# Kernel tuning notes

Hardware: AMD Instinct MI355X
Metric: run time of the kernel (lower is better)

## Reference

```python
import jax, jax.numpy as jnp
import numpy as np

N = 10000      # atoms
E = 160000     # edges (avg degree 16)
G = 20         # graphs
Z = 10         # num_elements
K = 64         # hidden scalar channels (hidden_irreps multiplicity)
NB = 8         # num_bessel
H = 64         # radial MLP width
LMAX = 3
LM = (LMAX + 1) ** 2   # 16 spherical-harmonic components
M = 16         # MLP_irreps width for final nonlinear readout
R_MAX = 5.0
AVG_NEIGH = 16.0
LS = np.array([l for l in range(LMAX + 1) for _ in range(2 * l + 1)])  # l index of each lm slot


def _sph(u):
    # real spherical harmonics up to l=3, 'component' normalization, on unit vectors u [E,3]
    x, y, z = u[:, 0], u[:, 1], u[:, 2]
    s3, s5, s15, s7 = 3.0 ** 0.5, 5.0 ** 0.5, 15.0 ** 0.5, 7.0 ** 0.5
    c31, c32, c33 = (21.0 / 8.0) ** 0.5, 105.0 ** 0.5, (35.0 / 8.0) ** 0.5
    Y = [jnp.ones_like(x),
         s3 * x, s3 * y, s3 * z,
         s15 * x * y, s15 * y * z, 0.5 * s5 * (3 * z * z - 1.0), s15 * x * z, 0.5 * s15 * (x * x - y * y),
         c33 * y * (3 * x * x - y * y), c32 * x * y * z, c31 * y * (5 * z * z - 1.0),
         0.5 * s7 * z * (5 * z * z - 3.0),
         c31 * x * (5 * z * z - 1.0), 0.5 * c32 * z * (x * x - y * y), c33 * x * (x * x - 3 * y * y)]
    return jnp.stack(Y, axis=-1)


def _radial(r):
    # Bessel radial basis with p=5 polynomial cutoff envelope
    u = r / R_MAX
    n = jnp.arange(1, NB + 1, dtype=r.dtype)
    bess = (2.0 / R_MAX) ** 0.5 * jnp.sin(n[None, :] * jnp.pi * u[:, None]) / r[:, None]
    env = jnp.where(u < 1.0, 1.0 - 21.0 * u ** 5 + 35.0 * u ** 6 - 15.0 * u ** 7, 0.0)
    return bess * env[:, None]


def _forward(node_attrs, positions, atomic_energies, W_embed, radial_W0, radial_W1, radial_W2, radial_W3, W_mix, Wz, W_out, w_read1, W_r1, w_r2, edge_index, batch):
    sender, receiver = edge_index[0], edge_index[1]
    vec = positions[receiver] - positions[sender]          # edge gather
    r = jnp.sqrt(jnp.sum(vec * vec, axis=-1) + 1e-12)
    Y = _sph(vec / r[:, None])                             # [E, 16]
    edge_feats = _radial(r)                                # [E, NB]
    node_e0 = node_attrs @ atomic_energies                 # [N]
    feats = node_attrs @ W_embed                           # node embedding [N, K]
    node_en = node_e0
    for t in range(2):  # num_interactions
        # radial MLP -> per-(channel,l) tensor-product weights
        h = edge_feats
        for W in (radial_W0[t], radial_W1[t], radial_W2[t]):
            h = jax.nn.silu(h @ W)
        Rw = (h @ radial_W3[t]).reshape(-1, K, LMAX + 1)[:, :, LS]   # [E, K, 16]
        # channelwise tensor product: sender feats x SH x radial weights
        msg = feats[sender][:, :, None] * Rw * Y[:, None, :]         # [E, K, 16]
        A = jax.ops.segment_sum(msg, receiver, num_segments=node_attrs.shape[0]) / AVG_NEIGH
        A = jnp.einsum('nkm,mkc->ncm', A, W_mix[t][LS])              # per-l linear channel mixing
        # equivariant product basis (correlation 3) -> invariant contractions with element-dep weights
        s1 = A[:, :, 0]
        inv2 = jnp.sum(A * A, axis=-1)
        b = (node_attrs @ Wz[t, 0]) * s1 + (node_attrs @ Wz[t, 1]) * inv2 + (node_attrs @ Wz[t, 2]) * (s1 * inv2)
        feats = b @ W_out[t]
        if t == 0:
            node_en = node_en + feats @ w_read1              # linear readout
        else:
            node_en = node_en + jax.nn.silu(feats @ W_r1) @ w_r2  # nonlinear readout
    return jax.ops.segment_sum(node_en, batch, num_segments=G)      # per-graph energies [G]


def setup_inputs():
    key = jax.random.key(0)
    ks = jax.random.split(key, 16)
    gn = lambda k, shape, fan: jax.random.normal(k, shape, dtype=jnp.float32) / (fan ** 0.5)
    species = jax.random.randint(ks[0], (N,), 0, Z)
    return {
        'node_attrs': jax.nn.one_hot(species, Z, dtype=jnp.float32),
        'positions': jax.random.normal(ks[1], (N, 3), dtype=jnp.float32) * 3.0,
        'edge_index': jax.random.randint(ks[2], (2, E), 0, N),
        'batch': jnp.sort(jax.random.randint(ks[3], (N,), 0, G)),
        'atomic_energies': jax.random.normal(ks[4], (Z,), dtype=jnp.float32),
        'W_embed': gn(ks[5], (Z, K), Z),
        'radial_W0': gn(ks[6], (2, NB, H), NB),
        'radial_W1': gn(ks[7], (2, H, H), H),
        'radial_W2': gn(ks[8], (2, H, H), H),
        'radial_W3': gn(ks[9], (2, H, K * (LMAX + 1)), H),
        'W_mix': gn(ks[10], (2, LMAX + 1, K, K), K),
        'Wz': gn(ks[11], (2, 3, Z, K), Z),
        'W_out': gn(ks[12], (2, K, K), K),
        'w_read1': gn(ks[13], (K,), K),
        'W_r1': gn(ks[14], (K, M), K),
        'w_r2': gn(ks[15], (M,), M),
    }


def reference(node_attrs, positions, edge_index, batch, atomic_energies, W_embed, radial_W0, radial_W1, radial_W2, radial_W3, W_mix, Wz, W_out, w_read1, W_r1, w_r2):
    return _forward(node_attrs, positions, atomic_energies, W_embed, radial_W0, radial_W1, radial_W2, radial_W3, W_mix, Wz, W_out, w_read1, W_r1, w_r2, edge_index, batch)
```

## Files before the change

kernel.cpp:

```cpp
#include <hip/hip_runtime.h>
#include <hip/hip_bf16.h>
#include <math.h>

#define NN 10000
#define NE 160000
#define NG 20
#define NZ 10
#define INV_AVG 0.0625f
#define PSTRIDE 76
#define NSTR 1040

typedef __attribute__((ext_vector_type(8))) short bf16x8;
typedef __attribute__((ext_vector_type(4))) float f32x4;
typedef __attribute__((ext_vector_type(4))) unsigned short u16x4;
typedef __attribute__((ext_vector_type(8))) unsigned short u16x8;

__device__ __forceinline__ float silu(float x) {
    return x * __builtin_amdgcn_rcpf(1.0f + __expf(-x));
}

__device__ __forceinline__ unsigned short f2b(float f) {
    union { float f; unsigned u; } v; v.f = f;
    unsigned r = v.u + 0x7FFF + ((v.u >> 16) & 1);
    return (unsigned short)(r >> 16);
}
__device__ __forceinline__ float b2f(unsigned short h) {
    union { unsigned u; float f; } v; v.u = ((unsigned)h) << 16; return v.f;
}

__global__ __launch_bounds__(256) void node_init(
    const float* __restrict__ attrs, const float* __restrict__ W_embed,
    const float* __restrict__ ae,
    float* __restrict__ feats, float* __restrict__ node_en)
{
    int gid = blockIdx.x * blockDim.x + threadIdx.x;
    if (gid >= NN * 64) return;
    int n = gid >> 6, k = gid & 63;
    float acc = 0.f;
#pragma unroll
    for (int z = 0; z < NZ; ++z) acc += attrs[n * NZ + z] * W_embed[z * 64 + k];
    feats[gid] = acc;
    if (k == 0) {
        float e0 = 0.f;
#pragma unroll
        for (int z = 0; z < NZ; ++z) e0 += attrs[n * NZ + z] * ae[z];
        node_en[n] = e0;
    }
}

__global__ __launch_bounds__(256) void csr_count(const int* __restrict__ ei, int* __restrict__ cnt)
{
    int e = blockIdx.x * 256 + threadIdx.x;
    if (e < NE) atomicAdd(&cnt[ei[NE + e]], 1);
}

__global__ __launch_bounds__(1024) void csr_scan(const int* __restrict__ cnt, int* __restrict__ row)
{
    __shared__ int part[1024];
    const int tid = threadIdx.x;
    const int base = tid * 10;
    int loc[10];
    int s = 0;
#pragma unroll
    for (int q = 0; q < 10; ++q) {
        int idx = base + q;
        int v = (idx < NN) ? cnt[idx] : 0;
        loc[q] = s; s += v;
    }
    part[tid] = s;
    __syncthreads();
    for (int off = 1; off < 1024; off <<= 1) {
        int v = (tid >= off) ? part[tid - off] : 0;
        __syncthreads();
        part[tid] += v;
        __syncthreads();
    }
    int pre = (tid > 0) ? part[tid - 1] : 0;
#pragma unroll
    for (int q = 0; q < 10; ++q) {
        int idx = base + q;
        if (idx < NN) row[idx] = pre + loc[q];
    }
    if (tid == 1023) row[NN] = part[1023];
}

__global__ __launch_bounds__(256) void csr_scatter(
    const int* __restrict__ ei, const int* __restrict__ row,
    int* __restrict__ cur, int* __restrict__ perm)
{
    int e = blockIdx.x * 256 + threadIdx.x;
    if (e < NE) {
        int r = ei[NE + e];
        int p = atomicAdd(&cur[r], 1);
        perm[row[r] + p] = e;
    }
}

__global__ __launch_bounds__(256) void w_prep(
    const float* __restrict__ rW0, const float* __restrict__ rW1,
    const float* __restrict__ rW2, const float* __restrict__ rW3,
    const float* __restrict__ Wmix,
    unsigned short* __restrict__ w0f, unsigned short* __restrict__ w1f,
    unsigned short* __restrict__ w2f, unsigned short* __restrict__ w3f,
    unsigned short* __restrict__ wmixf)
{
    int g = blockIdx.x * 256 + threadIdx.x;
    if (g < 4096) {
        int t = g >> 11, x = g & 2047;
        int nt = x >> 9, l = (x >> 3) & 63, j = x & 7;
        int k = (l >> 4) * 8 + j, c = nt * 16 + (l & 15);
        w0f[g] = (k < 8) ? f2b(rW0[t * 512 + k * 64 + c]) : (unsigned short)0;
    } else if (g < 20480) {
        int x0 = g - 4096;
        int t = x0 >> 13, x = x0 & 8191;
        int fidx = x >> 9, l = (x >> 3) & 63, j = x & 7;
        int kt = fidx >> 2, nt = fidx & 3;
        int k = kt * 32 + (l >> 4) * 8 + j, c = nt * 16 + (l & 15);
        w1f[x0] = f2b(rW1[t * 4096 + k * 64 + c]);
    } else if (g < 36864) {
        int x0 = g - 20480;
        int t = x0 >> 13, x = x0 & 8191;
        int fidx = x >> 9, l = (x >> 3) & 63, j = x & 7;
        int kt = fidx >> 2, nt = fidx & 3;
        int k = kt * 32 + (l >> 4) * 8 + j, c = nt * 16 + (l & 15);
        w2f[x0] = f2b(rW2[t * 4096 + k * 64 + c]);
    } else if (g < 69632) {
        int x0 = g - 36864;
        int t = x0 >> 14, x = x0 & 16383;
        int fidx = x >> 9, l = (x >> 3) & 63, j = x & 7;
        int kt = fidx >> 4, nt = fidx & 15;
        int k = kt * 32 + (l >> 4) * 8 + j, c = nt * 16 + (l & 15);
        w3f[x0] = f2b(rW3[t * 16384 + k * 256 + c]);
    } else if (g < 102400) {
        int x0 = g - 69632;
        int t = x0 >> 14;
        int x = x0 & 16383;
        int l = x >> 12;
        int xx = x & 4095;
        int f = xx >> 9, ll = (xx >> 3) & 63, j = xx & 7;
        int kt = f >> 2, ct = f & 3;
        int k = kt * 32 + (ll >> 4) * 8 + j, c = ct * 16 + (ll & 15);
        wmixf[x0] = f2b(Wmix[t * 16384 + l * 4096 + k * 64 + c]);
    }
}

__global__ __launch_bounds__(256) void edge_geom(
    const int* __restrict__ ei, const float* __restrict__ pos,
    const int* __restrict__ perm,
    unsigned short* __restrict__ ybg, unsigned short* __restrict__ ebg,
    int* __restrict__ snd_p)
{
    const int g = blockIdx.x * 256 + threadIdx.x;
    const int e = perm[g];
    const int snd = ei[e], rcv = ei[NE + e];
    snd_p[g] = snd;
    const float dx = pos[rcv * 3 + 0] - pos[snd * 3 + 0];
    const float dy = pos[rcv * 3 + 1] - pos[snd * 3 + 1];
    const float dz = pos[rcv * 3 + 2] - pos[snd * 3 + 2];
    const float r = sqrtf(dx * dx + dy * dy + dz * dz + 1e-12f);
    const float ir = 1.0f / r;
    const float x = dx * ir, y = dy * ir, z = dz * ir;
    const float xx = x * x, yy = y * y, zz = z * z;

    u16x8 ylo, yhi;
    ylo[0] = f2b(1.0f);
    ylo[1] = f2b(1.73205081f * x);
    ylo[2] = f2b(1.73205081f * y);
    ylo[3] = f2b(1.73205081f * z);
    ylo[4] = f2b(3.87298335f * x * y);
    ylo[5] = f2b(3.87298335f * y * z);
    ylo[6] = f2b(1.11803399f * (3.0f * zz - 1.0f));
    ylo[7] = f2b(3.87298335f * x * z);
    yhi[0] = f2b(1.93649167f * (xx - yy));
    yhi[1] = f2b(2.09165007f * y * (3.0f * xx - yy));
    yhi[2] = f2b(10.2469508f * x * y * z);
    yhi[3] = f2b(1.62018517f * y * (5.0f * zz - 1.0f));
    yhi[4] = f2b(1.32287566f * z * (5.0f * zz - 3.0f));
    yhi[5] = f2b(1.62018517f * x * (5.0f * zz - 1.0f));
    yhi[6] = f2b(5.12347538f * z * (xx - yy));
    yhi[7] = f2b(2.09165007f * x * (xx - 3.0f * yy));
    *(u16x8*)&ybg[(size_t)g * 16] = ylo;
    *(u16x8*)&ybg[(size_t)g * 16 + 8] = yhi;

    const float u = r * 0.2f;
    float env = 0.0f;
    if (u < 1.0f) {
        const float u2 = u * u, u5 = u2 * u2 * u;
        env = 1.0f - 21.0f * u5 + 35.0f * u5 * u - 15.0f * u5 * u2;
    }
    const float cb = 0.632455532f * ir * env;
    const float pu = 3.14159265358979f * u;
    u16x8 eb;
#pragma unroll
    for (int i = 0; i < 8; ++i) eb[i] = f2b(cb * __sinf((float)(i + 1) * pu));
    *(u16x8*)&ebg[(size_t)g * 8] = eb;
}

__global__ __launch_bounds__(256) void radial_fused(
    const unsigned short* __restrict__ ebg,
    const unsigned short* __restrict__ w0f,
    const unsigned short* __restrict__ w1f,
    const unsigned short* __restrict__ w2f,
    const unsigned short* __restrict__ w3f,
    unsigned short* __restrict__ rwb)
{
    __shared__ unsigned short sP[4][16 * PSTRIDE];
    const int w = threadIdx.x >> 6, lane = threadIdx.x & 63;
    const int tIdx = blockIdx.x * 4 + w;
    const int lg = lane >> 4, e16 = lane & 15;
    unsigned short* buf = &sP[w][0];

    const size_t g0 = (size_t)tIdx * 16;
    f32x4 c[4];

    bf16x8 a1 = {0, 0, 0, 0, 0, 0, 0, 0};
    if (lg == 0) a1 = *(const bf16x8*)&ebg[(g0 + e16) * 8];
#pragma unroll
    for (int nt = 0; nt < 4; ++nt) {
        const bf16x8 b = *(const bf16x8*)&w0f[nt * 512 + lane * 8];
        c[nt] = __builtin_amdgcn_mfma_f32_16x16x32_bf16(b, a1, (f32x4){0.f, 0.f, 0.f, 0.f}, 0, 0, 0);
    }
#pragma unroll
    for (int nt = 0; nt < 4; ++nt) {
        u16x4 o;
#pragma unroll
        for (int jj = 0; jj < 4; ++jj) o[jj] = f2b(silu(c[nt][jj]));
        *(u16x4*)&buf[e16 * PSTRIDE + nt * 16 + lg * 4] = o;
    }

    {
        const bf16x8 ak0 = *(const bf16x8*)&buf[e16 * PSTRIDE + lg * 8];
        const bf16x8 ak1 = *(const bf16x8*)&buf[e16 * PSTRIDE + 32 + lg * 8];
#pragma unroll
        for (int nt = 0; nt < 4; ++nt) {
            const bf16x8 b0 = *(const bf16x8*)&w1f[nt * 512 + lane * 8];
            const bf16x8 b1 = *(const bf16x8*)&w1f[(4 + nt) * 512 + lane * 8];
            f32x4 acc = __builtin_amdgcn_mfma_f32_16x16x32_bf16(b0, ak0, (f32x4){0.f, 0.f, 0.f, 0.f}, 0, 0, 0);
            c[nt] = __builtin_amdgcn_mfma_f32_16x16x32_bf16(b1, ak1, acc, 0, 0, 0);
        }
    }
#pragma unroll
    for (int nt = 0; nt < 4; ++nt) {
        u16x4 o;
#pragma unroll
        for (int jj = 0; jj < 4; ++jj) o[jj] = f2b(silu(c[nt][jj]));
        *(u16x4*)&buf[e16 * PSTRIDE + nt * 16 + lg * 4] = o;
    }

    {
        const bf16x8 ak0 = *(const bf16x8*)&buf[e16 * PSTRIDE + lg * 8];
        const bf16x8 ak1 = *(const bf16x8*)&buf[e16 * PSTRIDE + 32 + lg * 8];
#pragma unroll
        for (int nt = 0; nt < 4; ++nt) {
            const bf16x8 b0 = *(const bf16x8*)&w2f[nt * 512 + lane * 8];
            const bf16x8 b1 = *(const bf16x8*)&w2f[(4 + nt) * 512 + lane * 8];
            f32x4 acc = __builtin_amdgcn_mfma_f32_16x16x32_bf16(b0, ak0, (f32x4){0.f, 0.f, 0.f, 0.f}, 0, 0, 0);
            c[nt] = __builtin_amdgcn_mfma_f32_16x16x32_bf16(b1, ak1, acc, 0, 0, 0);
        }
    }
#pragma unroll
    for (int nt = 0; nt < 4; ++nt) {
        u16x4 o;
#pragma unroll
        for (int jj = 0; jj < 4; ++jj) o[jj] = f2b(silu(c[nt][jj]));
        *(u16x4*)&buf[e16 * PSTRIDE + nt * 16 + lg * 4] = o;
    }

    {
        const bf16x8 h0 = *(const bf16x8*)&buf[e16 * PSTRIDE + lg * 8];
        const bf16x8 h1 = *(const bf16x8*)&buf[e16 * PSTRIDE + 32 + lg * 8];
#pragma unroll 4
        for (int nt = 0; nt < 16; ++nt) {
            const bf16x8 b0 = *(const bf16x8*)&w3f[nt * 512 + lane * 8];
            const bf16x8 b1 = *(const bf16x8*)&w3f[(16 + nt) * 512 + lane * 8];
            f32x4 cc = __builtin_amdgcn_mfma_f32_16x16x32_bf16(b0, h0, (f32x4){0.f, 0.f, 0.f, 0.f}, 0, 0, 0);
            cc = __builtin_amdgcn_mfma_f32_16x16x32_bf16(b1, h1, cc, 0, 0, 0);
            u16x4 o;
#pragma unroll
            for (int jj = 0; jj < 4; ++jj) o[jj] = f2b(cc[jj]);
            *(u16x4*)&rwb[(g0 + e16) * 256 + nt * 16 + lg * 4] = o;
        }
    }
}

#define EDGE_FMA(rv_, f_, y0_, y1_) do { \
    const float p0 = (f_) * b2f((rv_)[0]), p1 = (f_) * b2f((rv_)[1]); \
    const float p2 = (f_) * b2f((rv_)[2]), p3 = (f_) * b2f((rv_)[3]); \
    acc[0]  += p0 * b2f((y0_)[0]); \
    acc[1]  += p1 * b2f((y0_)[1]);  acc[2]  += p1 * b2f((y0_)[2]);  acc[3]  += p1 * b2f((y0_)[3]); \
    acc[4]  += p2 * b2f((y0_)[4]);  acc[5]  += p2 * b2f((y0_)[5]);  acc[6]  += p2 * b2f((y0_)[6]); \
    acc[7]  += p2 * b2f((y0_)[7]);  acc[8]  += p2 * b2f((y1_)[0]); \
    acc[9]  += p3 * b2f((y1_)[1]);  acc[10] += p3 * b2f((y1_)[2]);  acc[11] += p3 * b2f((y1_)[3]); \
    acc[12] += p3 * b2f((y1_)[4]);  acc[13] += p3 * b2f((y1_)[5]);  acc[14] += p3 * b2f((y1_)[6]); \
    acc[15] += p3 * b2f((y1_)[7]); \
} while (0)

#define LOADBATCH(rv_, f_, y0_, y1_, gb_) do { \
    _Pragma("unroll") \
    for (int j = 0; j < 4; ++j) { \
        const int gg = (gb_) + j; \
        rv_[j] = *(const u16x4*)&rwb[(size_t)gg * 256 + lane * 4]; \
        f_[j]  = feats_in[(size_t)snd_p[gg] * 64 + lane]; \
        y0_[j] = *(const u16x8*)&ybg[(size_t)gg * 16]; \
        y1_[j] = *(const u16x8*)&ybg[(size_t)gg * 16 + 8]; \
    } } while (0)

#define FMABATCH(rv_, f_, y0_, y1_) do { \
    _Pragma("unroll") \
    for (int j = 0; j < 4; ++j) EDGE_FMA(rv_[j], f_[j], y0_[j], y1_[j]); } while (0)

__global__ __launch_bounds__(256) void msg_accum(
    const unsigned short* __restrict__ rwb, const unsigned short* __restrict__ ybg,
    const int* __restrict__ row, const int* __restrict__ snd_p,
    const float* __restrict__ feats_in, unsigned short* __restrict__ Abp)
{
    const int w = threadIdx.x >> 6, lane = threadIdx.x & 63;
    const int n = blockIdx.x * 4 + w;
    const int beg = row[n], end = row[n + 1];

    float acc[16];
#pragma unroll
    for (int m = 0; m < 16; ++m) acc[m] = 0.f;

    u16x4 rvA[4], rvB[4];
    float fA[4], fB[4];
    u16x8 y0A[4], y0B[4], y1A[4], y1B[4];

    const int nb = (end - beg) >> 2;
    if (nb > 0) {
        LOADBATCH(rvA, fA, y0A, y1A, beg);
        int b = 0;
        while (true) {
            if (b + 1 < nb) LOADBATCH(rvB, fB, y0B, y1B, beg + (b + 1) * 4);
            FMABATCH(rvA, fA, y0A, y1A);
            ++b;
            if (b >= nb) break;
            if (b + 1 < nb) LOADBATCH(rvA, fA, y0A, y1A, beg + (b + 1) * 4);
            FMABATCH(rvB, fB, y0B, y1B);
            ++b;
            if (b >= nb) break;
        }
    }
    for (int g = beg + nb * 4; g < end; ++g) {
        const u16x4 rv = *(const u16x4*)&rwb[(size_t)g * 256 + lane * 4];
        const float f = feats_in[(size_t)snd_p[g] * 64 + lane];
        const u16x8 y0 = *(const u16x8*)&ybg[(size_t)g * 16];
        const u16x8 y1 = *(const u16x8*)&ybg[(size_t)g * 16 + 8];
        EDGE_FMA(rv, f, y0, y1);
    }

#pragma unroll
    for (int m = 0; m < 16; ++m)
        Abp[(size_t)m * 640000 + (size_t)n * 64 + lane] = f2b(acc[m] * INV_AVG);
}

__global__ __launch_bounds__(256) void einsum_gate(
    const unsigned short* __restrict__ Abp,
    const unsigned short* __restrict__ wmixf,
    const float* __restrict__ attrs,
    const float* __restrict__ Wz, const float* __restrict__ Wout,
    const float* __restrict__ wread1, const float* __restrict__ Wr1,
    const float* __restrict__ wr2,
    float* __restrict__ feats_out, float* __restrict__ node_en, int t)
{
    __shared__ unsigned short sNew[16 * NSTR];
    __shared__ float sF[4][64];
    const int w = threadIdx.x >> 6, lane = threadIdx.x & 63;
    const int lg = lane >> 4, n16 = lane & 15;
    const size_t node0 = (size_t)blockIdx.x * 16;

#pragma unroll
    for (int q = 0; q < 4; ++q) {
        const int m = w * 4 + q;
        const int l = (m == 0) ? 0 : (m < 4) ? 1 : (m < 9) ? 2 : 3;
        const unsigned short* Am = Abp + (size_t)m * 640000;
        const bf16x8 a0 = *(const bf16x8*)&Am[(node0 + n16) * 64 + lg * 8];
        const bf16x8 a1 = *(const bf16x8*)&Am[(node0 + n16) * 64 + 32 + lg * 8];
        const unsigned short* Wl = wmixf + l * 4096;
#pragma unroll
        for (int ct = 0; ct < 4; ++ct) {
            const bf16x8 b0 = *(const bf16x8*)&Wl[ct * 512 + lane * 8];
            const bf16x8 b1 = *(const bf16x8*)&Wl[(4 + ct) * 512 + lane * 8];
            f32x4 cc = __builtin_amdgcn_mfma_f32_16x16x32_bf16(b0, a0, (f32x4){0.f, 0.f, 0.f, 0.f}, 0, 0, 0);
            cc = __builtin_amdgcn_mfma_f32_16x16x32_bf16(b1, a1, cc, 0, 0, 0);
            u16x4 o;
#pragma unroll
            for (int jj = 0; jj < 4; ++jj) o[jj] = f2b(cc[jj]);
            *(u16x4*)&sNew[n16 * NSTR + m * 64 + ct * 16 + lg * 4] = o;
        }
    }
    __syncthreads();

    for (int qq = 0; qq < 4; ++qq) {
        const int nl = w * 4 + qq;
        const int n = (int)node0 + nl;

        float vals[16];
#pragma unroll
        for (int m = 0; m < 16; ++m)
            vals[m] = b2f(sNew[nl * NSTR + m * 64 + lane]);

        const float s1 = vals[0];
        float inv2 = 0.f;
#pragma unroll
        for (int m = 0; m < 16; ++m) inv2 += vals[m] * vals[m];

        float z0 = 0.f, z1 = 0.f, z2 = 0.f;
#pragma unroll
        for (int zz = 0; zz < NZ; ++zz) {
            const float a = attrs[n * NZ + zz];
            z0 += a * Wz[(t * 3 + 0) * 640 + zz * 64 + lane];
            z1 += a * Wz[(t * 3 + 1) * 640 + zz * 64 + lane];
            z2 += a * Wz[(t * 3 + 2) * 640 + zz * 64 + lane];
        }
        const float b = z0 * s1 + z1 * inv2 + z2 * (s1 * inv2);

        sF[w][lane] = b;
        float fnew = 0.f;
#pragma unroll 8
        for (int j = 0; j < 64; ++j) fnew += sF[w][j] * Wout[j * 64 + lane];
        feats_out[(size_t)n * 64 + lane] = fnew;

        if (t == 0) {
            float v = fnew * wread1[lane];
#pragma unroll
            for (int off = 32; off > 0; off >>= 1) v += __shfl_down(v, off, 64);
            if (lane == 0) node_en[n] += v;
        } else {
            sF[w][lane] = fnew;
            if (lane < 16) {
                float a = 0.f;
#pragma unroll 8
                for (int j = 0; j < 64; ++j) a += sF[w][j] * Wr1[j * 16 + lane];
                float vv = silu(a) * wr2[lane];
                vv += __shfl_down(vv, 8, 64);
                vv += __shfl_down(vv, 4, 64);
                vv += __shfl_down(vv, 2, 64);
                vv += __shfl_down(vv, 1, 64);
                if (lane == 0) node_en[n] += vv;
            }
        }
    }
}

__global__ __launch_bounds__(1024) void final_reduce(
    const float* __restrict__ node_en, const int* __restrict__ batch,
    float* __restrict__ out)
{
    __shared__ float sg[NG];
    if (threadIdx.x < NG) sg[threadIdx.x] = 0.f;
    __syncthreads();
    for (int n = threadIdx.x; n < NN; n += 1024)
        atomicAdd(&sg[batch[n]], node_en[n]);
    __syncthreads();
    if (threadIdx.x < NG) out[threadIdx.x] = sg[threadIdx.x];
}

extern "C" void kernel_launch(void* const* d_in, const int* in_sizes, int n_in,
                              void* d_out, int out_size, void* d_ws, size_t ws_size,
                              hipStream_t stream) {
    const float* attrs   = (const float*)d_in[0];
    const float* pos     = (const float*)d_in[1];
    const int*   ei      = (const int*)d_in[2];
    const int*   batch   = (const int*)d_in[3];
    const float* ae      = (const float*)d_in[4];
    const float* W_embed = (const float*)d_in[5];
    const float* rW0     = (const float*)d_in[6];
    const float* rW1     = (const float*)d_in[7];
    const float* rW2     = (const float*)d_in[8];
    const float* rW3     = (const float*)d_in[9];
    const float* Wmix    = (const float*)d_in[10];
    const float* Wz      = (const float*)d_in[11];
    const float* Wout    = (const float*)d_in[12];
    const float* wread1  = (const float*)d_in[13];
    const float* Wr1     = (const float*)d_in[14];
    const float* wr2     = (const float*)d_in[15];
    float* out = (float*)d_out;

    char* ws = (char*)d_ws;
    unsigned short* rwb  = (unsigned short*)(ws);
    unsigned short* ybg  = (unsigned short*)(ws + 81920000);
    unsigned short* ebg  = (unsigned short*)(ws + 87040000);
    float* feats0        = (float*)(ws + 89600000);
    float* feats1        = (float*)(ws + 92160000);
    unsigned short* Abp  = (unsigned short*)(ws + 94720000);
    unsigned short* w0f  = (unsigned short*)(ws + 115200000);
    unsigned short* w1f  = (unsigned short*)(ws + 115208192);
    unsigned short* w2f  = (unsigned short*)(ws + 115240960);
    unsigned short* w3f  = (unsigned short*)(ws + 115273728);
    unsigned short* wmixf= (unsigned short*)(ws + 115339264);
    int* cnt             = (int*)(ws + 115404800);
    int* cur             = (int*)(ws + 115445760);
    int* rowst           = (int*)(ws + 115486720);
    int* perm            = (int*)(ws + 115527696);
    int* snd_p           = (int*)(ws + 116167696);
    float* node_en       = (float*)(ws + 116807696);

    hipMemsetAsync(cnt, 0, 81920, stream);

    node_init<<<2500, 256, 0, stream>>>(attrs, W_embed, ae, feats0, node_en);

    csr_count<<<625, 256, 0, stream>>>(ei, cnt);
    csr_scan<<<1, 1024, 0, stream>>>(cnt, rowst);
    csr_scatter<<<625, 256, 0, stream>>>(ei, rowst, cur, perm);

    w_prep<<<400, 256, 0, stream>>>(rW0, rW1, rW2, rW3, Wmix,
                                    w0f, w1f, w2f, w3f, wmixf);
    edge_geom<<<625, 256, 0, stream>>>(ei, pos, perm, ybg, ebg, snd_p);

    for (int t = 0; t < 2; ++t) {
        radial_fused<<<2500, 256, 0, stream>>>(
            ebg, w0f + t * 2048, w1f + t * 8192, w2f + t * 8192, w3f + t * 16384, rwb);
        msg_accum<<<2500, 256, 0, stream>>>(
            rwb, ybg, rowst, snd_p, (t == 0) ? feats0 : feats1, Abp);
        einsum_gate<<<625, 256, 0, stream>>>(
            Abp, wmixf + t * 16384, attrs, Wz, Wout + t * 4096,
            wread1, Wr1, wr2,
            (t == 0) ? feats1 : feats0, node_en, t);
    }
    final_reduce<<<1, 1024, 0, stream>>>(node_en, batch, out);
}
```

Before: 260.4 us.

## Co-schedule second-layer radial MLP with first message pass; merge setup kernels

The second interaction's radial MLP depends only on edge geometry, so it now runs inside the same launch as the first message accumulation, alternating blocks between the memory-bound gather and the MFMA-bound radial tile. This needs a second radial-weight buffer, which roughly doubles that workspace region. Setup kernels are also merged (node init with CSR count, scan with weight prep) to cut launch count and serialization. The aim is to overlap compute-heavy and memory-heavy work and remove small-kernel gaps, at the cost of extra workspace traffic and mixed-occupancy blocks.

```diff
diff --git a/kernel.cpp b/kernel.cpp
--- a/kernel.cpp
+++ b/kernel.cpp
@@ -28,75 +28,183 @@
     union { unsigned u; float f; } v; v.u = ((unsigned)h) << 16; return v.f;
 }
 
-__global__ __launch_bounds__(256) void node_init(
+__device__ __forceinline__ void radial_tile(
+    int tIdx, int lane, unsigned short* buf,
+    const unsigned short* __restrict__ ebg,
+    const unsigned short* __restrict__ w0f, const unsigned short* __restrict__ w1f,
+    const unsigned short* __restrict__ w2f, const unsigned short* __restrict__ w3f,
+    unsigned short* __restrict__ rwb)
+{
+    const int lg = lane >> 4, e16 = lane & 15;
+    const size_t g0 = (size_t)tIdx * 16;
+    f32x4 c[4];
+
+    bf16x8 a1 = {0, 0, 0, 0, 0, 0, 0, 0};
+    if (lg == 0) a1 = *(const bf16x8*)&ebg[(g0 + e16) * 8];
+#pragma unroll
+    for (int nt = 0; nt < 4; ++nt) {
+        const bf16x8 b = *(const bf16x8*)&w0f[nt * 512 + lane * 8];
+        c[nt] = __builtin_amdgcn_mfma_f32_16x16x32_bf16(b, a1, (f32x4){0.f, 0.f, 0.f, 0.f}, 0, 0, 0);
+    }
+#pragma unroll
+    for (int nt = 0; nt < 4; ++nt) {
+        u16x4 o;
+#pragma unroll
+        for (int jj = 0; jj < 4; ++jj) o[jj] = f2b(silu(c[nt][jj]));
+        *(u16x4*)&buf[e16 * PSTRIDE + nt * 16 + lg * 4] = o;
+    }
+
+    {
+        const bf16x8 ak0 = *(const bf16x8*)&buf[e16 * PSTRIDE + lg * 8];
+        const bf16x8 ak1 = *(const bf16x8*)&buf[e16 * PSTRIDE + 32 + lg * 8];
+#pragma unroll
+        for (int nt = 0; nt < 4; ++nt) {
+            const bf16x8 b0 = *(const bf16x8*)&w1f[nt * 512 + lane * 8];
+            const bf16x8 b1 = *(const bf16x8*)&w1f[(4 + nt) * 512 + lane * 8];
+            f32x4 acc = __builtin_amdgcn_mfma_f32_16x16x32_bf16(b0, ak0, (f32x4){0.f, 0.f, 0.f, 0.f}, 0, 0, 0);
+            c[nt] = __builtin_amdgcn_mfma_f32_16x16x32_bf16(b1, ak1, acc, 0, 0, 0);
+        }
+    }
+#pragma unroll
+    for (int nt = 0; nt < 4; ++nt) {
+        u16x4 o;
+#pragma unroll
+        for (int jj = 0; jj < 4; ++jj) o[jj] = f2b(silu(c[nt][jj]));
+        *(u16x4*)&buf[e16 * PSTRIDE + nt * 16 + lg * 4] = o;
+    }
+
+    {
+        const bf16x8 ak0 = *(const bf16x8*)&buf[e16 * PSTRIDE + lg * 8];
+        const bf16x8 ak1 = *(const bf16x8*)&buf[e16 * PSTRIDE + 32 + lg * 8];
+#pragma unroll
+        for (int nt = 0; nt < 4; ++nt) {
+            const bf16x8 b0 = *(const bf16x8*)&w2f[nt * 512 + lane * 8];
+            const bf16x8 b1 = *(const bf16x8*)&w2f[(4 + nt) * 512 + lane * 8];
+            f32x4 acc = __builtin_amdgcn_mfma_f32_16x16x32_bf16(b0, ak0, (f32x4){0.f, 0.f, 0.f, 0.f}, 0, 0, 0);
+            c[nt] = __builtin_amdgcn_mfma_f32_16x16x32_bf16(b1, ak1, acc, 0, 0, 0);
+        }
+    }
+#pragma unroll
+    for (int nt = 0; nt < 4; ++nt) {
+        u16x4 o;
+#pragma unroll
+        for (int jj = 0; jj < 4; ++jj) o[jj] = f2b(silu(c[nt][jj]));
+        *(u16x4*)&buf[e16 * PSTRIDE + nt * 16 + lg * 4] = o;
+    }
+
+    {
+        const bf16x8 h0 = *(const bf16x8*)&buf[e16 * PSTRIDE + lg * 8];
+        const bf16x8 h1 = *(const bf16x8*)&buf[e16 * PSTRIDE + 32 + lg * 8];
+#pragma unroll 4
+        for (int nt = 0; nt < 16; ++nt) {
+            const bf16x8 b0 = *(const bf16x8*)&w3f[nt * 512 + lane * 8];
+            const bf16x8 b1 = *(const bf16x8*)&w3f[(16 + nt) * 512 + lane * 8];
+            f32x4 cc = __builtin_amdgcn_mfma_f32_16x16x32_bf16(b0, h0, (f32x4){0.f, 0.f, 0.f, 0.f}, 0, 0, 0);
+            cc = __builtin_amdgcn_mfma_f32_16x16x32_bf16(b1, h1, cc, 0, 0, 0);
+            u16x4 o;
+#pragma unroll
+            for (int jj = 0; jj < 4; ++jj) o[jj] = f2b(cc[jj]);
+            *(u16x4*)&rwb[(g0 + e16) * 256 + nt * 16 + lg * 4] = o;
+        }
+    }
+}
+
+#define EDGE_FMA(rv_, f_, y0_, y1_) do { \
+    const float p0 = (f_) * b2f((rv_)[0]), p1 = (f_) * b2f((rv_)[1]); \
+    const float p2 = (f_) * b2f((rv_)[2]), p3 = (f_) * b2f((rv_)[3]); \
+    acc[0]  += p0 * b2f((y0_)[0]); \
+    acc[1]  += p1 * b2f((y0_)[1]);  acc[2]  += p1 * b2f((y0_)[2]);  acc[3]  += p1 * b2f((y0_)[3]); \
+    acc[4]  += p2 * b2f((y0_)[4]);  acc[5]  += p2 * b2f((y0_)[5]);  acc[6]  += p2 * b2f((y0_)[6]); \
+    acc[7]  += p2 * b2f((y0_)[7]);  acc[8]  += p2 * b2f((y1_)[0]); \
+    acc[9]  += p3 * b2f((y1_)[1]);  acc[10] += p3 * b2f((y1_)[2]);  acc[11] += p3 * b2f((y1_)[3]); \
+    acc[12] += p3 * b2f((y1_)[4]);  acc[13] += p3 * b2f((y1_)[5]);  acc[14] += p3 * b2f((y1_)[6]); \
+    acc[15] += p3 * b2f((y1_)[7]); \
+} while (0)
+
+#define LOADBATCH(rv_, f_, y0_, y1_, gb_) do { \
+    _Pragma("unroll") \
+    for (int j = 0; j < 4; ++j) { \
+        const int gg = (gb_) + j; \
+        rv_[j] = *(const u16x4*)&rwb[(size_t)gg * 256 + lane * 4]; \
+        f_[j]  = feats_in[(size_t)snd_p[gg] * 64 + lane]; \
+        y0_[j] = *(const u16x8*)&ybg[(size_t)gg * 16]; \
+        y1_[j] = *(const u16x8*)&ybg[(size_t)gg * 16 + 8]; \
+    } } while (0)
+
+#define FMABATCH(rv_, f_, y0_, y1_) do { \
+    _Pragma("unroll") \
+    for (int j = 0; j < 4; ++j) EDGE_FMA(rv_[j], f_[j], y0_[j], y1_[j]); } while (0)
+
+__device__ __forceinline__ void msg_node(
+    int n, int lane,
+    const unsigned short* __restrict__ rwb, const unsigned short* __restrict__ ybg,
+    const int* __restrict__ row, const int* __restrict__ snd_p,
+    const float* __restrict__ feats_in, unsigned short* __restrict__ Abp)
+{
+    const int beg = row[n], end = row[n + 1];
+
+    float acc[16];
+#pragma unroll
+    for (int m = 0; m < 16; ++m) acc[m] = 0.f;
+
+    u16x4 rvA[4], rvB[4];
+    float fA[4], fB[4];
+    u16x8 y0A[4], y0B[4], y1A[4], y1B[4];
+
+    const int nb = (end - beg) >> 2;
+    if (nb > 0) {
+        LOADBATCH(rvA, fA, y0A, y1A, beg);
+        int b = 0;
+        while (true) {
+            if (b + 1 < nb) LOADBATCH(rvB, fB, y0B, y1B, beg + (b + 1) * 4);
+            FMABATCH(rvA, fA, y0A, y1A);
+            ++b;
+            if (b >= nb) break;
+            if (b + 1 < nb) LOADBATCH(rvA, fA, y0A, y1A, beg + (b + 1) * 4);
+            FMABATCH(rvB, fB, y0B, y1B);
+            ++b;
+            if (b >= nb) break;
+        }
+    }
+    for (int g = beg + nb * 4; g < end; ++g) {
+        const u16x4 rv = *(const u16x4*)&rwb[(size_t)g * 256 + lane * 4];
+        const float f = feats_in[(size_t)snd_p[g] * 64 + lane];
+        const u16x8 y0 = *(const u16x8*)&ybg[(size_t)g * 16];
+        const u16x8 y1 = *(const u16x8*)&ybg[(size_t)g * 16 + 8];
+        EDGE_FMA(rv, f, y0, y1);
+    }
+
+#pragma unroll
+    for (int m = 0; m < 16; ++m)
+        Abp[(size_t)m * 640000 + (size_t)n * 64 + lane] = f2b(acc[m] * INV_AVG);
+}
+
+__global__ __launch_bounds__(256) void init_count(
     const float* __restrict__ attrs, const float* __restrict__ W_embed,
-    const float* __restrict__ ae,
-    float* __restrict__ feats, float* __restrict__ node_en)
-{
-    int gid = blockIdx.x * blockDim.x + threadIdx.x;
-    if (gid >= NN * 64) return;
-    int n = gid >> 6, k = gid & 63;
-    float acc = 0.f;
-#pragma unroll
-    for (int z = 0; z < NZ; ++z) acc += attrs[n * NZ + z] * W_embed[z * 64 + k];
-    feats[gid] = acc;
-    if (k == 0) {
-        float e0 = 0.f;
-#pragma unroll
-        for (int z = 0; z < NZ; ++z) e0 += attrs[n * NZ + z] * ae[z];
-        node_en[n] = e0;
-    }
-}
-
-__global__ __launch_bounds__(256) void csr_count(const int* __restrict__ ei, int* __restrict__ cnt)
-{
-    int e = blockIdx.x * 256 + threadIdx.x;
-    if (e < NE) atomicAdd(&cnt[ei[NE + e]], 1);
-}
-
-__global__ __launch_bounds__(1024) void csr_scan(const int* __restrict__ cnt, int* __restrict__ row)
-{
-    __shared__ int part[1024];
-    const int tid = threadIdx.x;
-    const int base = tid * 10;
-    int loc[10];
-    int s = 0;
-#pragma unroll
-    for (int q = 0; q < 10; ++q) {
-        int idx = base + q;
-        int v = (idx < NN) ? cnt[idx] : 0;
-        loc[q] = s; s += v;
-    }
-    part[tid] = s;
-    __syncthreads();
-    for (int off = 1; off < 1024; off <<= 1) {
-        int v = (tid >= off) ? part[tid - off] : 0;
-        __syncthreads();
-        part[tid] += v;
-        __syncthreads();
-    }
-    int pre = (tid > 0) ? part[tid - 1] : 0;
-#pragma unroll
-    for (int q = 0; q < 10; ++q) {
-        int idx = base + q;
-        if (idx < NN) row[idx] = pre + loc[q];
-    }
-    if (tid == 1023) row[NN] = part[1023];
-}
-
-__global__ __launch_bounds__(256) void csr_scatter(
-    const int* __restrict__ ei, const int* __restrict__ row,
-    int* __restrict__ cur, int* __restrict__ perm)
-{
-    int e = blockIdx.x * 256 + threadIdx.x;
-    if (e < NE) {
-        int r = ei[NE + e];
-        int p = atomicAdd(&cur[r], 1);
-        perm[row[r] + p] = e;
-    }
-}
-
-__global__ __launch_bounds__(256) void w_prep(
+    const float* __restrict__ ae, const int* __restrict__ ei,
+    float* __restrict__ feats, float* __restrict__ node_en, int* __restrict__ cnt)
+{
+    if (blockIdx.x < 2500) {
+        int gid = blockIdx.x * 256 + threadIdx.x;
+        int n = gid >> 6, k = gid & 63;
+        float acc = 0.f;
+#pragma unroll
+        for (int z = 0; z < NZ; ++z) acc += attrs[n * NZ + z] * W_embed[z * 64 + k];
+        feats[gid] = acc;
+        if (k == 0) {
+            float e0 = 0.f;
+#pragma unroll
+            for (int z = 0; z < NZ; ++z) e0 += attrs[n * NZ + z] * ae[z];
+            node_en[n] = e0;
+        }
+    } else {
+        int e = (blockIdx.x - 2500) * 256 + threadIdx.x;
+        if (e < NE) atomicAdd(&cnt[ei[NE + e]], 1);
+    }
+}
+
+__global__ __launch_bounds__(1024) void scan_prep(
+    const int* __restrict__ cnt, int* __restrict__ row,
     const float* __restrict__ rW0, const float* __restrict__ rW1,
     const float* __restrict__ rW2, const float* __restrict__ rW3,
     const float* __restrict__ Wmix,
@@ -104,43 +212,84 @@
     unsigned short* __restrict__ w2f, unsigned short* __restrict__ w3f,
     unsigned short* __restrict__ wmixf)
 {
-    int g = blockIdx.x * 256 + threadIdx.x;
-    if (g < 4096) {
-        int t = g >> 11, x = g & 2047;
-        int nt = x >> 9, l = (x >> 3) & 63, j = x & 7;
-        int k = (l >> 4) * 8 + j, c = nt * 16 + (l & 15);
-        w0f[g] = (k < 8) ? f2b(rW0[t * 512 + k * 64 + c]) : (unsigned short)0;
-    } else if (g < 20480) {
-        int x0 = g - 4096;
-        int t = x0 >> 13, x = x0 & 8191;
-        int fidx = x >> 9, l = (x >> 3) & 63, j = x & 7;
-        int kt = fidx >> 2, nt = fidx & 3;
-        int k = kt * 32 + (l >> 4) * 8 + j, c = nt * 16 + (l & 15);
-        w1f[x0] = f2b(rW1[t * 4096 + k * 64 + c]);
-    } else if (g < 36864) {
-        int x0 = g - 20480;
-        int t = x0 >> 13, x = x0 & 8191;
-        int fidx = x >> 9, l = (x >> 3) & 63, j = x & 7;
-        int kt = fidx >> 2, nt = fidx & 3;
-        int k = kt * 32 + (l >> 4) * 8 + j, c = nt * 16 + (l & 15);
-        w2f[x0] = f2b(rW2[t * 4096 + k * 64 + c]);
-    } else if (g < 69632) {
-        int x0 = g - 36864;
-        int t = x0 >> 14, x = x0 & 16383;
-        int fidx = x >> 9, l = (x >> 3) & 63, j = x & 7;
-        int kt = fidx >> 4, nt = fidx & 15;
-        int k = kt * 32 + (l >> 4) * 8 + j, c = nt * 16 + (l & 15);
-        w3f[x0] = f2b(rW3[t * 16384 + k * 256 + c]);
-    } else if (g < 102400) {
-        int x0 = g - 69632;
-        int t = x0 >> 14;
-        int x = x0 & 16383;
-        int l = x >> 12;
-        int xx = x & 4095;
-        int f = xx >> 9, ll = (xx >> 3) & 63, j = xx & 7;
-        int kt = f >> 2, ct = f & 3;
-        int k = kt * 32 + (ll >> 4) * 8 + j, c = ct * 16 + (ll & 15);
-        wmixf[x0] = f2b(Wmix[t * 16384 + l * 4096 + k * 64 + c]);
+    if (blockIdx.x == 0) {
+        __shared__ int part[1024];
+        const int tid = threadIdx.x;
+        const int base = tid * 10;
+        int loc[10];
+        int s = 0;
+#pragma unroll
+        for (int q = 0; q < 10; ++q) {
+            int idx = base + q;
+            int v = (idx < NN) ? cnt[idx] : 0;
+            loc[q] = s; s += v;
+        }
+        part[tid] = s;
+        __syncthreads();
+        for (int off = 1; off < 1024; off <<= 1) {
+            int v = (tid >= off) ? part[tid - off] : 0;
+            __syncthreads();
+            part[tid] += v;
+            __syncthreads();
+        }
+        int pre = (tid > 0) ? part[tid - 1] : 0;
+#pragma unroll
+        for (int q = 0; q < 10; ++q) {
+            int idx = base + q;
+            if (idx < NN) row[idx] = pre + loc[q];
+        }
+        if (tid == 1023) row[NN] = part[1023];
+    } else {
+        int g = (blockIdx.x - 1) * 1024 + threadIdx.x;
+        if (g < 4096) {
+            int t = g >> 11, x = g & 2047;
+            int nt = x >> 9, l = (x >> 3) & 63, j = x & 7;
+            int k = (l >> 4) * 8 + j, c = nt * 16 + (l & 15);
+            w0f[g] = (k < 8) ? f2b(rW0[t * 512 + k * 64 + c]) : (unsigned short)0;
+        } else if (g < 20480) {
+            int x0 = g - 4096;
+            int t = x0 >> 13, x = x0 & 8191;
+            int fidx = x >> 9, l = (x >> 3) & 63, j = x & 7;
+            int kt = fidx >> 2, nt = fidx & 3;
+            int k = kt * 32 + (l >> 4) * 8 + j, c = nt * 16 + (l & 15);
+            w1f[x0] = f2b(rW1[t * 4096 + k * 64 + c]);
+        } else if (g < 36864) {
+            int x0 = g - 20480;
+            int t = x0 >> 13, x = x0 & 8191;
+            int fidx = x >> 9, l = (x >> 3) & 63, j = x & 7;
+            int kt = fidx >> 2, nt = fidx & 3;
+            int k = kt * 32 + (l >> 4) * 8 + j, c = nt * 16 + (l & 15);
+            w2f[x0] = f2b(rW2[t * 4096 + k * 64 + c]);
+        } else if (g < 69632) {
+            int x0 = g - 36864;
+            int t = x0 >> 14, x = x0 & 16383;
+            int fidx = x >> 9, l = (x >> 3) & 63, j = x & 7;
+            int kt = fidx >> 4, nt = fidx & 15;
+            int k = kt * 32 + (l >> 4) * 8 + j, c = nt * 16 + (l & 15);
+            w3f[x0] = f2b(rW3[t * 16384 + k * 256 + c]);
+        } else if (g < 102400) {
+            int x0 = g - 69632;
+            int t = x0 >> 14;
+            int x = x0 & 16383;
+            int l = x >> 12;
+            int xx = x & 4095;
+            int f = xx >> 9, ll = (xx >> 3) & 63, j = xx & 7;
+            int kt = f >> 2, ct = f & 3;
+            int k = kt * 32 + (ll >> 4) * 8 + j, c = ct * 16 + (ll & 15);
+            wmixf[x0] = f2b(Wmix[t * 16384 + l * 4096 + k * 64 + c]);
+        }
+    }
+}
+
+__global__ __launch_bounds__(256) void csr_scatter(
+    const int* __restrict__ ei, const int* __restrict__ row,
+    int* __restrict__ cur, int* __restrict__ perm)
+{
+    int e = blockIdx.x * 256 + threadIdx.x;
+    if (e < NE) {
+        int r = ei[NE + e];
+        int p = atomicAdd(&cur[r], 1);
+        perm[row[r] + p] = e;
     }
 }
 
@@ -206,108 +355,27 @@
 {
     __shared__ unsigned short sP[4][16 * PSTRIDE];
     const int w = threadIdx.x >> 6, lane = threadIdx.x & 63;
-    const int tIdx = blockIdx.x * 4 + w;
-    const int lg = lane >> 4, e16 = lane & 15;
-    unsigned short* buf = &sP[w][0];
-
-    const size_t g0 = (size_t)tIdx * 16;
-    f32x4 c[4];
-
-    bf16x8 a1 = {0, 0, 0, 0, 0, 0, 0, 0};
-    if (lg == 0) a1 = *(const bf16x8*)&ebg[(g0 + e16) * 8];
-#pragma unroll
-    for (int nt = 0; nt < 4; ++nt) {
-        const bf16x8 b = *(const bf16x8*)&w0f[nt * 512 + lane * 8];
-        c[nt] = __builtin_amdgcn_mfma_f32_16x16x32_bf16(b, a1, (f32x4){0.f, 0.f, 0.f, 0.f}, 0, 0, 0);
-    }
-#pragma unroll
-    for (int nt = 0; nt < 4; ++nt) {
-        u16x4 o;
-#pragma unroll
-        for (int jj = 0; jj < 4; ++jj) o[jj] = f2b(silu(c[nt][jj]));
-        *(u16x4*)&buf[e16 * PSTRIDE + nt * 16 + lg * 4] = o;
-    }
-
-    {
-        const bf16x8 ak0 = *(const bf16x8*)&buf[e16 * PSTRIDE + lg * 8];
-        const bf16x8 ak1 = *(const bf16x8*)&buf[e16 * PSTRIDE + 32 + lg * 8];
-#pragma unroll
-        for (int nt = 0; nt < 4; ++nt) {
-            const bf16x8 b0 = *(const bf16x8*)&w1f[nt * 512 + lane * 8];
-            const bf16x8 b1 = *(const bf16x8*)&w1f[(4 + nt) * 512 + lane * 8];
-            f32x4 acc = __builtin_amdgcn_mfma_f32_16x16x32_bf16(b0, ak0, (f32x4){0.f, 0.f, 0.f, 0.f}, 0, 0, 0);
-            c[nt] = __builtin_amdgcn_mfma_f32_16x16x32_bf16(b1, ak1, acc, 0, 0, 0);
-        }
-    }
-#pragma unroll
-    for (int nt = 0; nt < 4; ++nt) {
-        u16x4 o;
-#pragma unroll
-        for (int jj = 0; jj < 4; ++jj) o[jj] = f2b(silu(c[nt][jj]));
-        *(u16x4*)&buf[e16 * PSTRIDE + nt * 16 + lg * 4] = o;
-    }
-
-    {
-        const bf16x8 ak0 = *(const bf16x8*)&buf[e16 * PSTRIDE + lg * 8];
-        const bf16x8 ak1 = *(const bf16x8*)&buf[e16 * PSTRIDE + 32 + lg * 8];
-#pragma unroll
-        for (int nt = 0; nt < 4; ++nt) {
-            const bf16x8 b0 = *(const bf16x8*)&w2f[nt * 512 + lane * 8];
-            const bf16x8 b1 = *(const bf16x8*)&w2f[(4 + nt) * 512 + lane * 8];
-            f32x4 acc = __builtin_amdgcn_mfma_f32_16x16x32_bf16(b0, ak0, (f32x4){0.f, 0.f, 0.f, 0.f}, 0, 0, 0);
-            c[nt] = __builtin_amdgcn_mfma_f32_16x16x32_bf16(b1, ak1, acc, 0, 0, 0);
-        }
-    }
-#pragma unroll
-    for (int nt = 0; nt < 4; ++nt) {
-        u16x4 o;
-#pragma unroll
-        for (int jj = 0; jj < 4; ++jj) o[jj] = f2b(silu(c[nt][jj]));
-        *(u16x4*)&buf[e16 * PSTRIDE + nt * 16 + lg * 4] = o;
-    }
-
-    {
-        const bf16x8 h0 = *(const bf16x8*)&buf[e16 * PSTRIDE + lg * 8];
-        const bf16x8 h1 = *(const bf16x8*)&buf[e16 * PSTRIDE + 32 + lg * 8];
-#pragma unroll 4
-        for (int nt = 0; nt < 16; ++nt) {
-            const bf16x8 b0 = *(const bf16x8*)&w3f[nt * 512 + lane * 8];
-            const bf16x8 b1 = *(const bf16x8*)&w3f[(16 + nt) * 512 + lane * 8];
-            f32x4 cc = __builtin_amdgcn_mfma_f32_16x16x32_bf16(b0, h0, (f32x4){0.f, 0.f, 0.f, 0.f}, 0, 0, 0);
-            cc = __builtin_amdgcn_mfma_f32_16x16x32_bf16(b1, h1, cc, 0, 0, 0);
-            u16x4 o;
-#pragma unroll
-            for (int jj = 0; jj < 4; ++jj) o[jj] = f2b(cc[jj]);
-            *(u16x4*)&rwb[(g0 + e16) * 256 + nt * 16 + lg * 4] = o;
-        }
-    }
-}
-
-#define EDGE_FMA(rv_, f_, y0_, y1_) do { \
-    const float p0 = (f_) * b2f((rv_)[0]), p1 = (f_) * b2f((rv_)[1]); \
-    const float p2 = (f_) * b2f((rv_)[2]), p3 = (f_) * b2f((rv_)[3]); \
-    acc[0]  += p0 * b2f((y0_)[0]); \
-    acc[1]  += p1 * b2f((y0_)[1]);  acc[2]  += p1 * b2f((y0_)[2]);  acc[3]  += p1 * b2f((y0_)[3]); \
-    acc[4]  += p2 * b2f((y0_)[4]);  acc[5]  += p2 * b2f((y0_)[5]);  acc[6]  += p2 * b2f((y0_)[6]); \
-    acc[7]  += p2 * b2f((y0_)[7]);  acc[8]  += p2 * b2f((y1_)[0]); \
-    acc[9]  += p3 * b2f((y1_)[1]);  acc[10] += p3 * b2f((y1_)[2]);  acc[11] += p3 * b2f((y1_)[3]); \
-    acc[12] += p3 * b2f((y1_)[4]);  acc[13] += p3 * b2f((y1_)[5]);  acc[14] += p3 * b2f((y1_)[6]); \
-    acc[15] += p3 * b2f((y1_)[7]); \
-} while (0)
-
-#define LOADBATCH(rv_, f_, y0_, y1_, gb_) do { \
-    _Pragma("unroll") \
-    for (int j = 0; j < 4; ++j) { \
-        const int gg = (gb_) + j; \
-        rv_[j] = *(const u16x4*)&rwb[(size_t)gg * 256 + lane * 4]; \
-        f_[j]  = feats_in[(size_t)snd_p[gg] * 64 + lane]; \
-        y0_[j] = *(const u16x8*)&ybg[(size_t)gg * 16]; \
-        y1_[j] = *(const u16x8*)&ybg[(size_t)gg * 16 + 8]; \
-    } } while (0)
-
-#define FMABATCH(rv_, f_, y0_, y1_) do { \
-    _Pragma("unroll") \
-    for (int j = 0; j < 4; ++j) EDGE_FMA(rv_[j], f_[j], y0_[j], y1_[j]); } while (0)
+    radial_tile(blockIdx.x * 4 + w, lane, &sP[w][0], ebg, w0f, w1f, w2f, w3f, rwb);
+}
+
+__global__ __launch_bounds__(256) void msg_radial(
+    const unsigned short* __restrict__ rwb0, const unsigned short* __restrict__ ybg,
+    const int* __restrict__ row, const int* __restrict__ snd_p,
+    const float* __restrict__ feats_in, unsigned short* __restrict__ Abp,
+    const unsigned short* __restrict__ ebg,
+    const unsigned short* __restrict__ w0f, const unsigned short* __restrict__ w1f,
+    const unsigned short* __restrict__ w2f, const unsigned short* __restrict__ w3f,
+    unsigned short* __restrict__ rwb1)
+{
+    __shared__ unsigned short sP[4][16 * PSTRIDE];
+    const int w = threadIdx.x >> 6, lane = threadIdx.x & 63;
+    const int sub = blockIdx.x >> 1;
+    if ((blockIdx.x & 1) == 0) {
+        msg_node(sub * 4 + w, lane, rwb0, ybg, row, snd_p, feats_in, Abp);
+    } else {
+        radial_tile(sub * 4 + w, lane, &sP[w][0], ebg, w0f, w1f, w2f, w3f, rwb1);
+    }
+}
 
 __global__ __launch_bounds__(256) void msg_accum(
     const unsigned short* __restrict__ rwb, const unsigned short* __restrict__ ybg,
@@ -315,43 +383,7 @@
     const float* __restrict__ feats_in, unsigned short* __restrict__ Abp)
 {
     const int w = threadIdx.x >> 6, lane = threadIdx.x & 63;
-    const int n = blockIdx.x * 4 + w;
-    const int beg = row[n], end = row[n + 1];
-
-    float acc[16];
-#pragma unroll
-    for (int m = 0; m < 16; ++m) acc[m] = 0.f;
-
-    u16x4 rvA[4], rvB[4];
-    float fA[4], fB[4];
-    u16x8 y0A[4], y0B[4], y1A[4], y1B[4];
-
-    const int nb = (end - beg) >> 2;
-    if (nb > 0) {
-        LOADBATCH(rvA, fA, y0A, y1A, beg);
-        int b = 0;
-        while (true) {
-            if (b + 1 < nb) LOADBATCH(rvB, fB, y0B, y1B, beg + (b + 1) * 4);
-            FMABATCH(rvA, fA, y0A, y1A);
-            ++b;
-            if (b >= nb) break;
-            if (b + 1 < nb) LOADBATCH(rvA, fA, y0A, y1A, beg + (b + 1) * 4);
-            FMABATCH(rvB, fB, y0B, y1B);
-            ++b;
-            if (b >= nb) break;
-        }
-    }
-    for (int g = beg + nb * 4; g < end; ++g) {
-        const u16x4 rv = *(const u16x4*)&rwb[(size_t)g * 256 + lane * 4];
-        const float f = feats_in[(size_t)snd_p[g] * 64 + lane];
-        const u16x8 y0 = *(const u16x8*)&ybg[(size_t)g * 16];
-        const u16x8 y1 = *(const u16x8*)&ybg[(size_t)g * 16 + 8];
-        EDGE_FMA(rv, f, y0, y1);
-    }
-
-#pragma unroll
-    for (int m = 0; m < 16; ++m)
-        Abp[(size_t)m * 640000 + (size_t)n * 64 + lane] = f2b(acc[m] * INV_AVG);
+    msg_node(blockIdx.x * 4 + w, lane, rwb, ybg, row, snd_p, feats_in, Abp);
 }
 
 __global__ __launch_bounds__(256) void einsum_gate(
@@ -478,45 +510,44 @@
     float* out = (float*)d_out;
 
     char* ws = (char*)d_ws;
-    unsigned short* rwb  = (unsigned short*)(ws);
-    unsigned short* ybg  = (unsigned short*)(ws + 81920000);
-    unsigned short* ebg  = (unsigned short*)(ws + 87040000);
-    float* feats0        = (float*)(ws + 89600000);
-    float* feats1        = (float*)(ws + 92160000);
-    unsigned short* Abp  = (unsigned short*)(ws + 94720000);
-    unsigned short* w0f  = (unsigned short*)(ws + 115200000);
-    unsigned short* w1f  = (unsigned short*)(ws + 115208192);
-    unsigned short* w2f  = (unsigned short*)(ws + 115240960);
-    unsigned short* w3f  = (unsigned short*)(ws + 115273728);
-    unsigned short* wmixf= (unsigned short*)(ws + 115339264);
-    int* cnt             = (int*)(ws + 115404800);
-    int* cur             = (int*)(ws + 115445760);
-    int* rowst           = (int*)(ws + 115486720);
-    int* perm            = (int*)(ws + 115527696);
-    int* snd_p           = (int*)(ws + 116167696);
-    float* node_en       = (float*)(ws + 116807696);
+    unsigned short* rwb0 = (unsigned short*)(ws);
+    unsigned short* rwb1 = (unsigned short*)(ws + 81920000);
+    unsigned short* ybg  = (unsigned short*)(ws + 163840000);
+    unsigned short* ebg  = (unsigned short*)(ws + 168960000);
+    float* feats0        = (float*)(ws + 171520000);
+    float* feats1        = (float*)(ws + 174080000);
+    unsigned short* Abp  = (unsigned short*)(ws + 176640000);
+    unsigned short* w0f  = (unsigned short*)(ws + 197120000);
+    unsigned short* w1f  = (unsigned short*)(ws + 197128192);
+    unsigned short* w2f  = (unsigned short*)(ws + 197160960);
+    unsigned short* w3f  = (unsigned short*)(ws + 197193728);
+    unsigned short* wmixf= (unsigned short*)(ws + 197259264);
+    int* cnt             = (int*)(ws + 197324800);
+    int* cur             = (int*)(ws + 197365760);
+    int* rowst           = (int*)(ws + 197406720);
+    int* perm            = (int*)(ws + 197447696);
+    int* snd_p           = (int*)(ws + 198087696);
+    float* node_en       = (float*)(ws + 198727696);
 
     hipMemsetAsync(cnt, 0, 81920, stream);
 
-    node_init<<<2500, 256, 0, stream>>>(attrs, W_embed, ae, feats0, node_en);
-
-    csr_count<<<625, 256, 0, stream>>>(ei, cnt);
-    csr_scan<<<1, 1024, 0, stream>>>(cnt, rowst);
+    init_count<<<3125, 256, 0, stream>>>(attrs, W_embed, ae, ei, feats0, node_en, cnt);
+    scan_prep<<<101, 1024, 0, stream>>>(cnt, rowst, rW0, rW1, rW2, rW3, Wmix,
+                                        w0f, w1f, w2f, w3f, wmixf);
     csr_scatter<<<625, 256, 0, stream>>>(ei, rowst, cur, perm);
-
-    w_prep<<<400, 256, 0, stream>>>(rW0, rW1, rW2, rW3, Wmix,
-                                    w0f, w1f, w2f, w3f, wmixf);
     edge_geom<<<625, 256, 0, stream>>>(ei, pos, perm, ybg, ebg, snd_p);
 
-    for (int t = 0; t < 2; ++t) {
-        radial_fused<<<2500, 256, 0, stream>>>(
-            ebg, w0f + t * 2048, w1f + t * 8192, w2f + t * 8192, w3f + t * 16384, rwb);
-        msg_accum<<<2500, 256, 0, stream>>>(
-            rwb, ybg, rowst, snd_p, (t == 0) ? feats0 : feats1, Abp);
-        einsum_gate<<<625, 256, 0, stream>>>(
-            Abp, wmixf + t * 16384, attrs, Wz, Wout + t * 4096,
-            wread1, Wr1, wr2,
-            (t == 0) ? feats1 : feats0, node_en, t);
-    }
+    radial_fused<<<2500, 256, 0, stream>>>(
+        ebg, w0f, w1f, w2f, w3f, rwb0);
+    msg_radial<<<5000, 256, 0, stream>>>(
+        rwb0, ybg, rowst, snd_p, feats0, Abp,
+        ebg, w0f + 2048, w1f + 8192, w2f + 8192, w3f + 16384, rwb1);
+    einsum_gate<<<625, 256, 0, stream>>>(
+        Abp, wmixf, attrs, Wz, Wout, wread1, Wr1, wr2, feats1, node_en, 0);
+    msg_accum<<<2500, 256, 0, stream>>>(
+        rwb1, ybg, rowst, snd_p, feats1, Abp);
+    einsum_gate<<<625, 256, 0, stream>>>(
+        Abp, wmixf + 16384, attrs, Wz, Wout + 4096, wread1, Wr1, wr2,
+        feats0, node_en, 1);
     final_reduce<<<1, 1024, 0, stream>>>(node_en, batch, out);
 }
```

Measured after the change: 266.6 us. 2.4% more time.
